# Kernel optimization log

Hardware: AMD Instinct MI355X
Metric: run time of the kernel (lower is better)

The kernel has to match this reference:

```python
import jax, jax.numpy as jnp
import numpy as np

B, NQ, NK, D, H, DFF = 4, 1024, 1024, 1024, 16, 4096
DH = D // H
SCALE = 1.0 / np.sqrt(D).astype(np.float32)  # torch code scales by sqrt(dim_V), not head_dim
LN_EPS = 1e-5


def setup_inputs() -> dict:
    key = jax.random.key(0)
    ks = jax.random.split(key, 20)
    s = lambda fan_in: 1.0 / np.sqrt(fan_in).astype(np.float32)
    inp = {
        "Q": jax.random.normal(ks[0], (B, NQ, D), jnp.float32),
        "K": jax.random.normal(ks[1], (B, NK, D), jnp.float32),
        # attention projections (torch Linear stored here as [in, out])
        "Wq": jax.random.uniform(ks[2], (D, D), jnp.float32, -s(D), s(D)),
        "bq": jnp.zeros((D,), jnp.float32),
        "Wk": jax.random.uniform(ks[3], (D, D), jnp.float32, -s(D), s(D)),
        "bk": jnp.zeros((D,), jnp.float32),
        "Wv": jax.random.uniform(ks[4], (D, D), jnp.float32, -s(D), s(D)),
        "bv": jnp.zeros((D,), jnp.float32),
        "Wo": jax.random.uniform(ks[5], (D, D), jnp.float32, -s(D), s(D)),
        "bo": jnp.zeros((D,), jnp.float32),
        # FFN
        "W1": jax.random.uniform(ks[6], (D, DFF), jnp.float32, -s(D), s(D)),
        "b1": jnp.zeros((DFF,), jnp.float32),
        "W2": jax.random.uniform(ks[7], (DFF, D), jnp.float32, -s(DFF), s(DFF)),
        "b2": jnp.zeros((D,), jnp.float32),
        # LayerNorms
        "g0": jnp.ones((D,), jnp.float32),
        "be0": jnp.zeros((D,), jnp.float32),
        "g1": jnp.ones((D,), jnp.float32),
        "be1": jnp.zeros((D,), jnp.float32),
    }
    return inp


def _layernorm(x, g, b):
    mu = x.mean(-1, keepdims=True)
    var = ((x - mu) ** 2).mean(-1, keepdims=True)
    return (x - mu) * jax.lax.rsqrt(var + LN_EPS) * g + b


def reference(Q, K, Wq, bq, Wk, bk, Wv, bv, Wo, bo, W1, b1, W2, b2, g0, be0, g1, be1):
    # multi-head attention (MHA path, mask=None)
    q = (Q @ Wq + bq).reshape(B, NQ, H, DH)
    k = (K @ Wk + bk).reshape(B, NK, H, DH)
    v = (K @ Wv + bv).reshape(B, NK, H, DH)
    E = jnp.einsum("bqhd,bkhd->bhqk", q, k) * SCALE  # [B,H,NQ,NK]
    A = jax.nn.softmax(E, axis=-1)
    O = jnp.einsum("bhqk,bkhd->bqhd", A, v).reshape(B, NQ, D)
    O = O @ Wo + bo
    # residual + LN0
    X = _layernorm(Q + O, g0, be0)
    # FFN + residual + LN1
    Y = jnp.maximum(X @ W1 + b1, 0.0) @ W2 + b2
    return _layernorm(X + Y, g1, be1)
```

## Files before the change

kernel.cpp:

```cpp
#include <hip/hip_runtime.h>
#include <math.h>

#define B_   4
#define NQ_  1024
#define NK_  1024
#define D_   1024
#define H_   16
#define DH_  64
#define DFF_ 4096
#define SCALE_ (1.0f/32.0f)
#define LN_EPS_ 1e-5f

typedef __attribute__((ext_vector_type(8))) short bf16x8_t;
typedef __attribute__((ext_vector_type(4))) float f32x4_t;

__device__ __forceinline__ ushort f2bf_rne(float x) {
    unsigned u = __float_as_uint(x);
    unsigned r = (u + 0x7FFFu + ((u >> 16) & 1u)) >> 16;
    return (ushort)r;
}
__device__ __forceinline__ float bf2f(ushort h) {
    return __uint_as_float(((unsigned)h) << 16);
}

__device__ __forceinline__ void gl_lds16(const ushort* g, ushort* l) {
    __builtin_amdgcn_global_load_lds(
        (const __attribute__((address_space(1))) unsigned int*)g,
        (__attribute__((address_space(3))) unsigned int*)l, 16, 0, 0);
}

__global__ __launch_bounds__(256) void split_rows(const float* __restrict__ src,
        ushort* __restrict__ hi, ushort* __restrict__ lo, int n4)
{
    int i = blockIdx.x * 256 + threadIdx.x;
    if (i >= n4) return;
    float4 v = ((const float4*)src)[i];
    ushort4 h, l;
    h.x = f2bf_rne(v.x); l.x = f2bf_rne(v.x - bf2f(h.x));
    h.y = f2bf_rne(v.y); l.y = f2bf_rne(v.y - bf2f(h.y));
    h.z = f2bf_rne(v.z); l.z = f2bf_rne(v.z - bf2f(h.z));
    h.w = f2bf_rne(v.w); l.w = f2bf_rne(v.w - bf2f(h.w));
    ((ushort4*)hi)[i] = h;
    ((ushort4*)lo)[i] = l;
}

__global__ __launch_bounds__(256) void split_tr(const float* __restrict__ Wsrc,
        ushort* __restrict__ th, ushort* __restrict__ tl, int K, int N)
{
    __shared__ float tile[32][33];
    const int nb = blockIdx.x * 32, kb = blockIdx.y * 32;
    const int t = threadIdx.x;
    {
        int r = t >> 3, c4 = (t & 7) * 4;
        float4 v = *(const float4*)&Wsrc[(size_t)(kb + r) * N + nb + c4];
        tile[r][c4 + 0] = v.x; tile[r][c4 + 1] = v.y;
        tile[r][c4 + 2] = v.z; tile[r][c4 + 3] = v.w;
    }
    __syncthreads();
    {
        int n = t >> 3, k4 = (t & 7) * 4;
        float a0 = tile[k4 + 0][n], a1 = tile[k4 + 1][n];
        float a2 = tile[k4 + 2][n], a3 = tile[k4 + 3][n];
        ushort4 h, l;
        h.x = f2bf_rne(a0); l.x = f2bf_rne(a0 - bf2f(h.x));
        h.y = f2bf_rne(a1); l.y = f2bf_rne(a1 - bf2f(h.y));
        h.z = f2bf_rne(a2); l.z = f2bf_rne(a2 - bf2f(h.z));
        h.w = f2bf_rne(a3); l.w = f2bf_rne(a3 - bf2f(h.w));
        size_t o = (size_t)(nb + n) * K + kb + k4;
        *(ushort4*)&th[o] = h;
        *(ushort4*)&tl[o] = l;
    }
}

template<bool RELU, int OMODE>
__device__ __forceinline__ void gemm_body(
        const ushort* __restrict__ Ah, const ushort* __restrict__ Al,
        const ushort* __restrict__ Bh, const ushort* __restrict__ Bl,
        const float* __restrict__ bias,
        float* __restrict__ C, ushort* __restrict__ Ch, ushort* __restrict__ Cl,
        int M, int N, int Kd, int Klen, int brow, int bcol)
{
    __shared__ __align__(16) ushort S[2][4][128 * 32];

    const int t    = threadIdx.x;
    const int lane = t & 63;
    const int w    = t >> 6;
    const int wr   = (w >> 1) * 64;
    const int wc   = (w & 1) * 64;
    const int fr   = lane & 15;
    const int g    = lane >> 4;
    const int sS   = ((g ^ ((fr >> 1) & 3)) << 3);
    const int cl   = lane & 15;
    const int rq   = (lane >> 4) * 4;

    float bpre[4];
    #pragma unroll
    for (int j = 0; j < 4; ++j)
        bpre[j] = bias ? bias[bcol + wc + j * 16 + cl] : 0.f;

    f32x4_t acc[4][4];
    #pragma unroll
    for (int i = 0; i < 4; ++i)
        #pragma unroll
        for (int j = 0; j < 4; ++j)
            acc[i][j] = (f32x4_t){0.f, 0.f, 0.f, 0.f};

    const int lrow  = lane >> 2;
    const int lslot = ((lane & 3) ^ ((lane >> 3) & 3)) << 3;
    const int c0    = w * 2;

    auto issue2 = [&](const ushort* gpp, int rb, int pl, int buf, int k0) {
        #pragma unroll
        for (int ii = 0; ii < 2; ++ii) {
            int c = c0 + ii;
            gl_lds16(gpp + (size_t)(rb + c * 16 + lrow) * Kd + k0 + lslot,
                     &S[buf][pl][c * 512]);
        }
    };

    bf16x8_t ahf[4], bhf[4], blf[4], alf[4];

    issue2(Ah, brow, 0, 0, 0);
    issue2(Bh, bcol, 2, 0, 0);
    issue2(Bl, bcol, 3, 0, 0);
    issue2(Al, brow, 1, 0, 0);
    asm volatile("s_waitcnt vmcnt(4)" ::: "memory");
    __builtin_amdgcn_s_barrier();

    const int NT = Klen >> 5;
    for (int tt = 0; tt < NT; ++tt) {
        const int cur = tt & 1, nxt = cur ^ 1;
        const int kn  = (tt + 1) << 5;
        const bool more = (tt + 1 < NT);

        #pragma unroll
        for (int i = 0; i < 4; ++i)
            ahf[i] = *(const bf16x8_t*)&S[cur][0][(wr + i * 16 + fr) * 32 + sS];
        #pragma unroll
        for (int j = 0; j < 4; ++j)
            bhf[j] = *(const bf16x8_t*)&S[cur][2][(wc + j * 16 + fr) * 32 + sS];
        if (more) {
            issue2(Ah, brow, 0, nxt, kn);
            issue2(Bh, bcol, 2, nxt, kn);
            asm volatile("s_waitcnt vmcnt(6)" ::: "memory");
        } else {
            asm volatile("s_waitcnt vmcnt(2)" ::: "memory");
        }
        __builtin_amdgcn_s_barrier();
        asm volatile("s_waitcnt lgkmcnt(0)" ::: "memory");
        __builtin_amdgcn_sched_barrier(0);
        __builtin_amdgcn_s_setprio(1);
        #pragma unroll
        for (int i = 0; i < 4; ++i)
            #pragma unroll
            for (int j = 0; j < 4; ++j)
                acc[i][j] = __builtin_amdgcn_mfma_f32_16x16x32_bf16(ahf[i], bhf[j], acc[i][j], 0, 0, 0);
        __builtin_amdgcn_s_setprio(0);
        __builtin_amdgcn_s_barrier();

        #pragma unroll
        for (int j = 0; j < 4; ++j)
            blf[j] = *(const bf16x8_t*)&S[cur][3][(wc + j * 16 + fr) * 32 + sS];
        if (more) {
            issue2(Bl, bcol, 3, nxt, kn);
            asm volatile("s_waitcnt vmcnt(6)" ::: "memory");
        } else {
            asm volatile("s_waitcnt vmcnt(0)" ::: "memory");
        }
        __builtin_amdgcn_s_barrier();
        asm volatile("s_waitcnt lgkmcnt(0)" ::: "memory");
        __builtin_amdgcn_sched_barrier(0);
        __builtin_amdgcn_s_setprio(1);
        #pragma unroll
        for (int i = 0; i < 4; ++i)
            #pragma unroll
            for (int j = 0; j < 4; ++j)
                acc[i][j] = __builtin_amdgcn_mfma_f32_16x16x32_bf16(ahf[i], blf[j], acc[i][j], 0, 0, 0);
        __builtin_amdgcn_s_setprio(0);
        __builtin_amdgcn_s_barrier();

        #pragma unroll
        for (int i = 0; i < 4; ++i)
            alf[i] = *(const bf16x8_t*)&S[cur][1][(wr + i * 16 + fr) * 32 + sS];
        if (more) {
            issue2(Al, brow, 1, nxt, kn);
            asm volatile("s_waitcnt vmcnt(4)" ::: "memory");
        }
        __builtin_amdgcn_s_barrier();
        asm volatile("s_waitcnt lgkmcnt(0)" ::: "memory");
        __builtin_amdgcn_sched_barrier(0);
        __builtin_amdgcn_s_setprio(1);
        #pragma unroll
        for (int i = 0; i < 4; ++i)
            #pragma unroll
            for (int j = 0; j < 4; ++j)
                acc[i][j] = __builtin_amdgcn_mfma_f32_16x16x32_bf16(alf[i], bhf[j], acc[i][j], 0, 0, 0);
        __builtin_amdgcn_s_setprio(0);
        __builtin_amdgcn_s_barrier();
    }

    if (OMODE == 0) {
        #pragma unroll
        for (int j = 0; j < 4; ++j) {
            int col = bcol + wc + j * 16 + cl;
            #pragma unroll
            for (int i = 0; i < 4; ++i)
                #pragma unroll
                for (int r = 0; r < 4; ++r) {
                    int row = brow + wr + i * 16 + rq + r;
                    float v = acc[i][j][r] + bpre[j];
                    if (RELU) v = fmaxf(v, 0.f);
                    C[(size_t)row * N + col] = v;
                }
        }
    } else {
        float* E = (float*)&S[0][0][0] + w * 4096;
        #pragma unroll
        for (int j = 0; j < 4; ++j) {
            #pragma unroll
            for (int i = 0; i < 4; ++i)
                #pragma unroll
                for (int r = 0; r < 4; ++r) {
                    float v = acc[i][j][r] + bpre[j];
                    if (RELU) v = fmaxf(v, 0.f);
                    E[(i * 16 + rq + r) * 64 + j * 16 + cl] = v;
                }
        }
        __syncthreads();
        const int rr8 = lane >> 3;
        const int c8  = (lane & 7) * 8;
        #pragma unroll
        for (int p = 0; p < 8; ++p) {
            int rl = p * 8 + rr8;
            float4 va = *(float4*)&E[rl * 64 + c8];
            float4 vb = *(float4*)&E[rl * 64 + c8 + 4];
            float v[8] = {va.x, va.y, va.z, va.w, vb.x, vb.y, vb.z, vb.w};
            bf16x8_t hv, lv;
            #pragma unroll
            for (int q = 0; q < 8; ++q) {
                ushort hh = f2bf_rne(v[q]);
                hv[q] = (short)hh;
                lv[q] = (short)f2bf_rne(v[q] - bf2f(hh));
            }
            size_t o = (size_t)(brow + wr + rl) * N + (bcol + wc + c8);
            *(bf16x8_t*)&Ch[o] = hv;
            if (OMODE == 1) *(bf16x8_t*)&Cl[o] = lv;
        }
    }
}

__device__ __forceinline__ void swz_block(int& brow, int& bcol, int tile) {
    const int nx  = gridDim.x;
    const int lin = blockIdx.y * nx + blockIdx.x;
    const int cpx = (nx * gridDim.y) >> 3;
    const int swz = (lin & 7) * cpx + (lin >> 3);
    brow = (swz / nx) * tile;
    bcol = (swz % nx) * tile;
}

template<bool RELU, int OMODE>
__global__ __launch_bounds__(256) void gemm_mfma(
        const ushort* __restrict__ Ah, const ushort* __restrict__ Al,
        const ushort* __restrict__ Bh, const ushort* __restrict__ Bl,
        const float* __restrict__ bias,
        float* __restrict__ C, ushort* __restrict__ Ch, ushort* __restrict__ Cl,
        int M, int N, int Kd)
{
    int brow, bcol;
    swz_block(brow, bcol, 128);
    gemm_body<RELU, OMODE>(Ah, Al, Bh, Bl, bias, C, Ch, Cl, M, N, Kd, Kd, brow, bcol);
}

__global__ __launch_bounds__(256) void gemm_splitk2(
        const ushort* __restrict__ Ah, const ushort* __restrict__ Al,
        const ushort* __restrict__ Bh, const ushort* __restrict__ Bl,
        const float* __restrict__ bias,
        float* __restrict__ C0, float* __restrict__ C1,
        int M, int N, int Kd)
{
    int brow, bcol;
    swz_block(brow, bcol, 128);
    const int z = blockIdx.z;
    const int Kh2 = Kd >> 1;
    const int ko  = z * Kh2;
    gemm_body<false, 0>(Ah + ko, Al + ko, Bh + ko, Bl + ko,
                        z == 0 ? bias : nullptr,
                        z == 0 ? C0 : C1, nullptr, nullptr,
                        M, N, Kd, Kh2, brow, bcol);
}

struct QkvArgs {
    const ushort* Ah[3]; const ushort* Al[3];
    const ushort* Bh[3]; const ushort* Bl[3];
    const float*  bias[3];
    ushort*       Co[3];
};

__global__ __launch_bounds__(256) void gemm_qkv(QkvArgs qa, int M, int N, int Kd)
{
    int brow, bcol;
    swz_block(brow, bcol, 128);
    const int z = blockIdx.z;
    gemm_body<false, 2>(qa.Ah[z], qa.Al[z], qa.Bh[z], qa.Bl[z], qa.bias[z],
                        nullptr, qa.Co[z], nullptr, M, N, Kd, Kd, brow, bcol);
}

__global__ __launch_bounds__(256) void flash_attn_mfma(
        const ushort* __restrict__ qh, const ushort* __restrict__ kh,
        const ushort* __restrict__ vh,
        ushort* __restrict__ Oh, ushort* __restrict__ Ol)
{
    __shared__ __align__(16) ushort sk[32 * 72];
    __shared__ __align__(16) ushort svt[64 * 40];
    __shared__ __align__(16) ushort pbuf[4][16 * 40];

    const int bid  = blockIdx.x;
    const int slot = bid >> 3;
    const int bh   = (bid & 7) * 8 + (slot >> 4);
    const int qt   = slot & 15;
    const int b    = bh >> 4;
    const int h    = bh & 15;
    const int qb   = qt * 64;

    const int t = threadIdx.x, lane = t & 63, w = t >> 6;
    const int l15 = lane & 15, g = lane >> 4;

    bf16x8_t qf[2];
    {
        size_t qrow = ((size_t)(b * NQ_) + qb + w * 16 + l15) * D_ + h * DH_;
        qf[0] = *(const bf16x8_t*)&qh[qrow + 0  + 8 * g];
        qf[1] = *(const bf16x8_t*)&qh[qrow + 32 + 8 * g];
    }

    f32x4_t acc[4];
    #pragma unroll
    for (int dt = 0; dt < 4; ++dt) acc[dt] = (f32x4_t){0.f, 0.f, 0.f, 0.f};
    float m[4]    = {-INFINITY, -INFINITY, -INFINITY, -INFINITY};
    float lsum[4] = {0.f, 0.f, 0.f, 0.f};

    const int kkv = t >> 3,  kds = (t & 7) * 8;
    const int vkv = t & 31,  vds = (t >> 5) * 8;
    const size_t kvbase = (size_t)(b * NK_) * D_ + h * DH_;

    for (int kt = 0; kt < NK_; kt += 32) {
        __syncthreads();
        {
            bf16x8_t kk = *(const bf16x8_t*)&kh[kvbase + (size_t)(kt + kkv) * D_ + kds];
            *(bf16x8_t*)&sk[kkv * 72 + kds] = kk;
            bf16x8_t vv = *(const bf16x8_t*)&vh[kvbase + (size_t)(kt + vkv) * D_ + vds];
            #pragma unroll
            for (int j = 0; j < 8; ++j)
                svt[(vds + j) * 40 + vkv] = (ushort)vv[j];
        }
        __syncthreads();

        f32x4_t s0 = (f32x4_t){0.f,0.f,0.f,0.f};
        f32x4_t s1 = (f32x4_t){0.f,0.f,0.f,0.f};
        #pragma unroll
        for (int c = 0; c < 2; ++c) {
            bf16x8_t k0 = *(const bf16x8_t*)&sk[(l15     ) * 72 + 32 * c + 8 * g];
            bf16x8_t k1 = *(const bf16x8_t*)&sk[(l15 + 16) * 72 + 32 * c + 8 * g];
            s0 = __builtin_amdgcn_mfma_f32_16x16x32_bf16(qf[c], k0, s0, 0, 0, 0);
            s1 = __builtin_amdgcn_mfma_f32_16x16x32_bf16(qf[c], k1, s1, 0, 0, 0);
        }

        float p0[4], p1[4], corr[4];
        #pragma unroll
        for (int r = 0; r < 4; ++r) {
            float e0 = s0[r] * SCALE_, e1 = s1[r] * SCALE_;
            float tm = fmaxf(e0, e1);
            tm = fmaxf(tm, __shfl_xor(tm, 1, 64));
            tm = fmaxf(tm, __shfl_xor(tm, 2, 64));
            tm = fmaxf(tm, __shfl_xor(tm, 4, 64));
            tm = fmaxf(tm, __shfl_xor(tm, 8, 64));
            float mn = fmaxf(m[r], tm);
            corr[r] = __expf(m[r] - mn);
            p0[r] = __expf(e0 - mn);
            p1[r] = __expf(e1 - mn);
            float ps = p0[r] + p1[r];
            ps += __shfl_xor(ps, 1, 64);
            ps += __shfl_xor(ps, 2, 64);
            ps += __shfl_xor(ps, 4, 64);
            ps += __shfl_xor(ps, 8, 64);
            lsum[r] = lsum[r] * corr[r] + ps;
            m[r] = mn;
        }
        #pragma unroll
        for (int dt = 0; dt < 4; ++dt)
            #pragma unroll
            for (int r = 0; r < 4; ++r)
                acc[dt][r] *= corr[r];

        ushort* pw = &pbuf[w][0];
        #pragma unroll
        for (int r = 0; r < 4; ++r) {
            pw[(4 * g + r) * 40 + l15     ] = f2bf_rne(p0[r]);
            pw[(4 * g + r) * 40 + l15 + 16] = f2bf_rne(p1[r]);
        }
        bf16x8_t pa = *(const bf16x8_t*)&pw[l15 * 40 + 8 * g];

        #pragma unroll
        for (int dt = 0; dt < 4; ++dt) {
            bf16x8_t vf = *(const bf16x8_t*)&svt[(16 * dt + l15) * 40 + 8 * g];
            acc[dt] = __builtin_amdgcn_mfma_f32_16x16x32_bf16(pa, vf, acc[dt], 0, 0, 0);
        }
    }

    float inv[4];
    #pragma unroll
    for (int r = 0; r < 4; ++r) inv[r] = 1.0f / lsum[r];
    #pragma unroll
    for (int dt = 0; dt < 4; ++dt) {
        #pragma unroll
        for (int r = 0; r < 4; ++r) {
            int row = b * NQ_ + qb + w * 16 + 4 * g + r;
            int col = h * DH_ + 16 * dt + l15;
            float v = acc[dt][r] * inv[r];
            ushort hh = f2bf_rne(v);
            Oh[(size_t)row * D_ + col] = hh;
            Ol[(size_t)row * D_ + col] = f2bf_rne(v - bf2f(hh));
        }
    }
}

template<bool SPLIT>
__global__ __launch_bounds__(256) void add_ln3(const float* __restrict__ a0,
        const float* __restrict__ a1, const float* __restrict__ r,
        const float* __restrict__ g, const float* __restrict__ be,
        float* __restrict__ out, ushort* __restrict__ oh, ushort* __restrict__ ol)
{
    const int row = blockIdx.x;
    const int t = threadIdx.x;
    float vals[4];
    float s1 = 0.0f, s2 = 0.0f;
    #pragma unroll
    for (int i = 0; i < 4; ++i) {
        int col = t + i * 256;
        size_t o = (size_t)row * D_ + col;
        float vv = a0[o] + a1[o] + r[o];
        vals[i] = vv;
        s1 += vv;
        s2 += vv * vv;
    }
    #pragma unroll
    for (int off = 32; off > 0; off >>= 1) {
        s1 += __shfl_down(s1, off, 64);
        s2 += __shfl_down(s2, off, 64);
    }
    __shared__ float p1[4], p2[4];
    const int wave = t >> 6;
    if ((t & 63) == 0) { p1[wave] = s1; p2[wave] = s2; }
    __syncthreads();
    s1 = p1[0] + p1[1] + p1[2] + p1[3];
    s2 = p2[0] + p2[1] + p2[2] + p2[3];
    const float mean = s1 * (1.0f / D_);
    const float var  = s2 * (1.0f / D_) - mean * mean;
    const float rstd = rsqrtf(var + LN_EPS_);
    #pragma unroll
    for (int i = 0; i < 4; ++i) {
        int col = t + i * 256;
        float v = (vals[i] - mean) * rstd * g[col] + be[col];
        out[(size_t)row * D_ + col] = v;
        if (SPLIT) {
            ushort h = f2bf_rne(v);
            oh[(size_t)row * D_ + col] = h;
            ol[(size_t)row * D_ + col] = f2bf_rne(v - bf2f(h));
        }
    }
}

extern "C" void kernel_launch(void* const* d_in, const int* in_sizes, int n_in,
                              void* d_out, int out_size, void* d_ws, size_t ws_size,
                              hipStream_t stream)
{
    const float* Q   = (const float*)d_in[0];
    const float* K   = (const float*)d_in[1];
    const float* Wq  = (const float*)d_in[2];
    const float* bq  = (const float*)d_in[3];
    const float* Wk  = (const float*)d_in[4];
    const float* bk  = (const float*)d_in[5];
    const float* Wv  = (const float*)d_in[6];
    const float* bv  = (const float*)d_in[7];
    const float* Wo  = (const float*)d_in[8];
    const float* bo  = (const float*)d_in[9];
    const float* W1  = (const float*)d_in[10];
    const float* b1  = (const float*)d_in[11];
    const float* W2  = (const float*)d_in[12];
    const float* b2  = (const float*)d_in[13];
    const float* g0  = (const float*)d_in[14];
    const float* be0 = (const float*)d_in[15];
    const float* g1  = (const float*)d_in[16];
    const float* be1 = (const float*)d_in[17];

    unsigned char* Wb = (unsigned char*)d_ws;
    const size_t MBy = 1ull << 20;

    ushort* Qh   = (ushort*)(Wb +  0 * MBy);
    ushort* Ql   = (ushort*)(Wb +  8 * MBy);
    ushort* Kh   = (ushort*)(Wb + 16 * MBy);
    ushort* Kl   = (ushort*)(Wb + 24 * MBy);
    ushort* Wqh  = (ushort*)(Wb + 32 * MBy);
    ushort* Wql  = (ushort*)(Wb + 34 * MBy);
    ushort* Wkh  = (ushort*)(Wb + 36 * MBy);
    ushort* Wkl  = (ushort*)(Wb + 38 * MBy);
    ushort* Wvh  = (ushort*)(Wb + 40 * MBy);
    ushort* Wvl  = (ushort*)(Wb + 42 * MBy);
    ushort* Woh  = (ushort*)(Wb + 44 * MBy);
    ushort* Wol  = (ushort*)(Wb + 46 * MBy);
    ushort* qhp  = (ushort*)(Wb + 48 * MBy);
    ushort* khp  = (ushort*)(Wb + 56 * MBy);
    ushort* vhp  = (ushort*)(Wb + 64 * MBy);
    ushort* aOh  = (ushort*)(Wb + 72 * MBy);
    ushort* aOl  = (ushort*)(Wb + 80 * MBy);

    float*  oprj0 = (float*)(Wb + 16 * MBy);
    float*  oprj1 = (float*)(Wb + 56 * MBy);
    float*  Xf    = (float*)(Wb +  0 * MBy);
    ushort* Xh    = (ushort*)(Wb + 32 * MBy);
    ushort* Xl    = (ushort*)(Wb + 40 * MBy);
    ushort* W1h   = (ushort*)(Wb + 16 * MBy);
    ushort* W1l   = (ushort*)(Wb + 24 * MBy);
    ushort* Hih   = (ushort*)(Wb + 80 * MBy);
    ushort* Hil   = (ushort*)(Wb + 48 * MBy);
    ushort* W2h   = (ushort*)(Wb + 16 * MBy);
    ushort* W2l   = (ushort*)(Wb + 24 * MBy);
    float*  Y0    = (float*)(Wb + 32 * MBy);
    float*  Y1    = (float*)d_out;

    const int M = B_ * NQ_;
    const int n4act = M * D_ / 4;
    dim3 blk(256);
    dim3 gQKV(D_ / 128, M / 128, 3);
    dim3 gSK(D_ / 128, M / 128, 2);
    dim3 gF(DFF_ / 128, M / 128);

    split_rows<<<n4act / 256, blk, 0, stream>>>(Q, Qh, Ql, n4act);
    split_rows<<<n4act / 256, blk, 0, stream>>>(K, Kh, Kl, n4act);
    split_tr<<<dim3(D_/32, D_/32), blk, 0, stream>>>(Wq, Wqh, Wql, D_, D_);
    split_tr<<<dim3(D_/32, D_/32), blk, 0, stream>>>(Wk, Wkh, Wkl, D_, D_);
    split_tr<<<dim3(D_/32, D_/32), blk, 0, stream>>>(Wv, Wvh, Wvl, D_, D_);
    split_tr<<<dim3(D_/32, D_/32), blk, 0, stream>>>(Wo, Woh, Wol, D_, D_);

    QkvArgs qa;
    qa.Ah[0] = Qh;  qa.Al[0] = Ql;  qa.Bh[0] = Wqh; qa.Bl[0] = Wql; qa.bias[0] = bq; qa.Co[0] = qhp;
    qa.Ah[1] = Kh;  qa.Al[1] = Kl;  qa.Bh[1] = Wkh; qa.Bl[1] = Wkl; qa.bias[1] = bk; qa.Co[1] = khp;
    qa.Ah[2] = Kh;  qa.Al[2] = Kl;  qa.Bh[2] = Wvh; qa.Bl[2] = Wvl; qa.bias[2] = bv; qa.Co[2] = vhp;
    gemm_qkv<<<gQKV, blk, 0, stream>>>(qa, M, D_, D_);

    flash_attn_mfma<<<dim3(1024), blk, 0, stream>>>(qhp, khp, vhp, aOh, aOl);

    gemm_splitk2<<<gSK, blk, 0, stream>>>(aOh, aOl, Woh, Wol, bo, oprj0, oprj1, M, D_, D_);
    add_ln3<true><<<M, blk, 0, stream>>>(oprj0, oprj1, Q, g0, be0, Xf, Xh, Xl);

    split_tr<<<dim3(DFF_/32, D_/32), blk, 0, stream>>>(W1, W1h, W1l, D_, DFF_);
    gemm_mfma<true,1><<<gF, blk, 0, stream>>>(Xh, Xl, W1h, W1l, b1, nullptr, Hih, Hil, M, DFF_, D_);
    split_tr<<<dim3(D_/32, DFF_/32), blk, 0, stream>>>(W2, W2h, W2l, DFF_, D_);

    gemm_splitk2<<<gSK, blk, 0, stream>>>(Hih, Hil, W2h, W2l, b2, Y0, Y1, M, D_, DFF_);
    add_ln3<false><<<M, blk, 0, stream>>>(Y0, Y1, Xf, g1, be1, (float*)d_out, nullptr, nullptr);
}
```

Baseline: 453.1 us.

## Transpose attention MFMAs, prefetch K/V to registers, vectorize P and output stores

The flash attention kernel swaps MFMA operand order so each lane owns a single query row. The softmax max and sum then reduce with two cross-group shuffles instead of four per row, and each lane keeps one running max and sum. Next K/V tiles are prefetched into registers while the current tile is being computed, and P is written to LDS as packed 4-element vectors. The output is staged through shared memory so the hi/lo bf16 results go out as 16-byte vector stores instead of scattered 2-byte stores. This costs more shared memory (8192 shorts) and more registers for the prefetch.

```diff
diff --git a/kernel.cpp b/kernel.cpp
--- a/kernel.cpp
+++ b/kernel.cpp
@@ -310,9 +310,10 @@
         const ushort* __restrict__ vh,
         ushort* __restrict__ Oh, ushort* __restrict__ Ol)
 {
-    __shared__ __align__(16) ushort sk[32 * 72];
-    __shared__ __align__(16) ushort svt[64 * 40];
-    __shared__ __align__(16) ushort pbuf[4][16 * 40];
+    __shared__ __align__(16) ushort SMEM[8192];
+    ushort* sk  = SMEM;
+    ushort* svt = SMEM + 2304;
+    ushort* pw0 = SMEM + 4864;
 
     const int bid  = blockIdx.x;
     const int slot = bid >> 3;
@@ -335,24 +336,28 @@
     f32x4_t acc[4];
     #pragma unroll
     for (int dt = 0; dt < 4; ++dt) acc[dt] = (f32x4_t){0.f, 0.f, 0.f, 0.f};
-    float m[4]    = {-INFINITY, -INFINITY, -INFINITY, -INFINITY};
-    float lsum[4] = {0.f, 0.f, 0.f, 0.f};
+    float m = -INFINITY, l = 0.0f;
 
     const int kkv = t >> 3,  kds = (t & 7) * 8;
     const int vkv = t & 31,  vds = (t >> 5) * 8;
     const size_t kvbase = (size_t)(b * NK_) * D_ + h * DH_;
 
+    bf16x8_t kreg = *(const bf16x8_t*)&kh[kvbase + (size_t)kkv * D_ + kds];
+    bf16x8_t vreg = *(const bf16x8_t*)&vh[kvbase + (size_t)vkv * D_ + vds];
+
+    ushort* pw = pw0 + w * 640;
+
     for (int kt = 0; kt < NK_; kt += 32) {
         __syncthreads();
-        {
-            bf16x8_t kk = *(const bf16x8_t*)&kh[kvbase + (size_t)(kt + kkv) * D_ + kds];
-            *(bf16x8_t*)&sk[kkv * 72 + kds] = kk;
-            bf16x8_t vv = *(const bf16x8_t*)&vh[kvbase + (size_t)(kt + vkv) * D_ + vds];
-            #pragma unroll
-            for (int j = 0; j < 8; ++j)
-                svt[(vds + j) * 40 + vkv] = (ushort)vv[j];
-        }
+        *(bf16x8_t*)&sk[kkv * 72 + kds] = kreg;
+        #pragma unroll
+        for (int j = 0; j < 8; ++j)
+            svt[(vds + j) * 40 + vkv] = (ushort)vreg[j];
         __syncthreads();
+        if (kt + 32 < NK_) {
+            kreg = *(const bf16x8_t*)&kh[kvbase + (size_t)(kt + 32 + kkv) * D_ + kds];
+            vreg = *(const bf16x8_t*)&vh[kvbase + (size_t)(kt + 32 + vkv) * D_ + vds];
+        }
 
         f32x4_t s0 = (f32x4_t){0.f,0.f,0.f,0.f};
         f32x4_t s1 = (f32x4_t){0.f,0.f,0.f,0.f};
@@ -360,67 +365,79 @@
         for (int c = 0; c < 2; ++c) {
             bf16x8_t k0 = *(const bf16x8_t*)&sk[(l15     ) * 72 + 32 * c + 8 * g];
             bf16x8_t k1 = *(const bf16x8_t*)&sk[(l15 + 16) * 72 + 32 * c + 8 * g];
-            s0 = __builtin_amdgcn_mfma_f32_16x16x32_bf16(qf[c], k0, s0, 0, 0, 0);
-            s1 = __builtin_amdgcn_mfma_f32_16x16x32_bf16(qf[c], k1, s1, 0, 0, 0);
-        }
-
-        float p0[4], p1[4], corr[4];
+            s0 = __builtin_amdgcn_mfma_f32_16x16x32_bf16(k0, qf[c], s0, 0, 0, 0);
+            s1 = __builtin_amdgcn_mfma_f32_16x16x32_bf16(k1, qf[c], s1, 0, 0, 0);
+        }
+
+        float e0[4], e1[4];
+        #pragma unroll
+        for (int r = 0; r < 4; ++r) { e0[r] = s0[r] * SCALE_; e1[r] = s1[r] * SCALE_; }
+        float tmax = fmaxf(fmaxf(fmaxf(e0[0], e0[1]), fmaxf(e0[2], e0[3])),
+                           fmaxf(fmaxf(e1[0], e1[1]), fmaxf(e1[2], e1[3])));
+        tmax = fmaxf(tmax, __shfl_xor(tmax, 16, 64));
+        tmax = fmaxf(tmax, __shfl_xor(tmax, 32, 64));
+        float mn   = fmaxf(m, tmax);
+        float corr = __expf(m - mn);
+        float p0[4], p1[4];
+        float ps = 0.f;
         #pragma unroll
         for (int r = 0; r < 4; ++r) {
-            float e0 = s0[r] * SCALE_, e1 = s1[r] * SCALE_;
-            float tm = fmaxf(e0, e1);
-            tm = fmaxf(tm, __shfl_xor(tm, 1, 64));
-            tm = fmaxf(tm, __shfl_xor(tm, 2, 64));
-            tm = fmaxf(tm, __shfl_xor(tm, 4, 64));
-            tm = fmaxf(tm, __shfl_xor(tm, 8, 64));
-            float mn = fmaxf(m[r], tm);
-            corr[r] = __expf(m[r] - mn);
-            p0[r] = __expf(e0 - mn);
-            p1[r] = __expf(e1 - mn);
-            float ps = p0[r] + p1[r];
-            ps += __shfl_xor(ps, 1, 64);
-            ps += __shfl_xor(ps, 2, 64);
-            ps += __shfl_xor(ps, 4, 64);
-            ps += __shfl_xor(ps, 8, 64);
-            lsum[r] = lsum[r] * corr[r] + ps;
-            m[r] = mn;
-        }
+            p0[r] = __expf(e0[r] - mn);
+            p1[r] = __expf(e1[r] - mn);
+            ps += p0[r] + p1[r];
+        }
+        ps += __shfl_xor(ps, 16, 64);
+        ps += __shfl_xor(ps, 32, 64);
+        l = l * corr + ps;
+        m = mn;
         #pragma unroll
         for (int dt = 0; dt < 4; ++dt)
             #pragma unroll
             for (int r = 0; r < 4; ++r)
-                acc[dt][r] *= corr[r];
-
-        ushort* pw = &pbuf[w][0];
-        #pragma unroll
-        for (int r = 0; r < 4; ++r) {
-            pw[(4 * g + r) * 40 + l15     ] = f2bf_rne(p0[r]);
-            pw[(4 * g + r) * 40 + l15 + 16] = f2bf_rne(p1[r]);
-        }
+                acc[dt][r] *= corr;
+
+        ushort4 pk0, pk1;
+        pk0.x = f2bf_rne(p0[0]); pk0.y = f2bf_rne(p0[1]);
+        pk0.z = f2bf_rne(p0[2]); pk0.w = f2bf_rne(p0[3]);
+        pk1.x = f2bf_rne(p1[0]); pk1.y = f2bf_rne(p1[1]);
+        pk1.z = f2bf_rne(p1[2]); pk1.w = f2bf_rne(p1[3]);
+        *(ushort4*)&pw[l15 * 40 + 4 * g]      = pk0;
+        *(ushort4*)&pw[l15 * 40 + 16 + 4 * g] = pk1;
         bf16x8_t pa = *(const bf16x8_t*)&pw[l15 * 40 + 8 * g];
 
         #pragma unroll
         for (int dt = 0; dt < 4; ++dt) {
             bf16x8_t vf = *(const bf16x8_t*)&svt[(16 * dt + l15) * 40 + 8 * g];
-            acc[dt] = __builtin_amdgcn_mfma_f32_16x16x32_bf16(pa, vf, acc[dt], 0, 0, 0);
-        }
-    }
-
-    float inv[4];
-    #pragma unroll
-    for (int r = 0; r < 4; ++r) inv[r] = 1.0f / lsum[r];
-    #pragma unroll
-    for (int dt = 0; dt < 4; ++dt) {
-        #pragma unroll
-        for (int r = 0; r < 4; ++r) {
-            int row = b * NQ_ + qb + w * 16 + 4 * g + r;
-            int col = h * DH_ + 16 * dt + l15;
-            float v = acc[dt][r] * inv[r];
-            ushort hh = f2bf_rne(v);
-            Oh[(size_t)row * D_ + col] = hh;
-            Ol[(size_t)row * D_ + col] = f2bf_rne(v - bf2f(hh));
-        }
-    }
+            acc[dt] = __builtin_amdgcn_mfma_f32_16x16x32_bf16(vf, pa, acc[dt], 0, 0, 0);
+        }
+    }
+
+    __syncthreads();
+    float invl = 1.0f / l;
+    float* Ew = (float*)SMEM + w * 1024;
+    #pragma unroll
+    for (int dt = 0; dt < 4; ++dt)
+        #pragma unroll
+        for (int r = 0; r < 4; ++r)
+            Ew[(16 * dt + 4 * g + r) * 16 + l15] = acc[dt][r] * invl;
+    const int ql = lane >> 2;
+    const int dc = (lane & 3) * 16;
+    float ov[16];
+    #pragma unroll
+    for (int j = 0; j < 16; ++j) ov[j] = Ew[(dc + j) * 16 + ql];
+    bf16x8_t hv0, hv1, lv0, lv1;
+    #pragma unroll
+    for (int j = 0; j < 8; ++j) {
+        ushort ha = f2bf_rne(ov[j]);
+        ushort hb = f2bf_rne(ov[8 + j]);
+        hv0[j] = (short)ha; lv0[j] = (short)f2bf_rne(ov[j] - bf2f(ha));
+        hv1[j] = (short)hb; lv1[j] = (short)f2bf_rne(ov[8 + j] - bf2f(hb));
+    }
+    size_t orow = ((size_t)(b * NQ_) + qb + w * 16 + ql) * D_ + h * DH_ + dc;
+    *(bf16x8_t*)&Oh[orow]     = hv0;
+    *(bf16x8_t*)&Oh[orow + 8] = hv1;
+    *(bf16x8_t*)&Ol[orow]     = lv0;
+    *(bf16x8_t*)&Ol[orow + 8] = lv1;
 }
 
 template<bool SPLIT>
```

New measurement: 413.3 us. 1.1x faster.
